# Optimization experiments

Hardware: AMD Instinct MI355X
Metric: run time of the kernel (lower is better)

## Reference

```python
import jax, jax.numpy as jnp
import numpy as np

DIM = 1024
HEADS = 16
HEAD_DIM = DIM // HEADS
HIDDEN = 4 * DIM
EPS = 1e-5


def layernorm(x, g, b):
    mu = jnp.mean(x, axis=-1, keepdims=True)
    var = jnp.var(x, axis=-1, keepdims=True)
    return (x - mu) * jax.lax.rsqrt(var + EPS) * g + b


def setup_inputs() -> dict:
    key = jax.random.key(0)
    ks = jax.random.split(key, 6)
    B, N = 4, 1024
    s = lambda fan_in: 1.0 / np.sqrt(fan_in)
    return {
        "x": jax.random.normal(ks[0], (B, N, DIM), jnp.float32),
        "ln1_g": jnp.ones((DIM,), jnp.float32),
        "ln1_b": jnp.zeros((DIM,), jnp.float32),
        "qkv_w": jax.random.normal(ks[1], (3 * DIM, DIM), jnp.float32) * s(DIM),
        "qkv_b": jnp.zeros((3 * DIM,), jnp.float32),
        "proj_w": jax.random.normal(ks[2], (DIM, DIM), jnp.float32) * s(DIM),
        "proj_b": jnp.zeros((DIM,), jnp.float32),
        "ln2_g": jnp.ones((DIM,), jnp.float32),
        "ln2_b": jnp.zeros((DIM,), jnp.float32),
        "fc1_w": jax.random.normal(ks[3], (HIDDEN, DIM), jnp.float32) * s(DIM),
        "fc1_b": jnp.zeros((HIDDEN,), jnp.float32),
        "fc2_w": jax.random.normal(ks[4], (DIM, HIDDEN), jnp.float32) * s(HIDDEN),
        "fc2_b": jnp.zeros((DIM,), jnp.float32),
    }


def reference(x, ln1_g, ln1_b, qkv_w, qkv_b, proj_w, proj_b,
              ln2_g, ln2_b, fc1_w, fc1_b, fc2_w, fc2_b):
    B, N, C = x.shape
    scale = HEAD_DIM ** -0.5

    # --- attention branch ---
    h = layernorm(x, ln1_g, ln1_b)
    qkv = h @ qkv_w.T + qkv_b                      # [B,N,3C]
    qkv = qkv.reshape(B, N, 3, HEADS, HEAD_DIM)
    q = qkv[:, :, 0].transpose(0, 2, 1, 3) * scale  # [B,H,N,D]
    k = qkv[:, :, 1].transpose(0, 2, 1, 3)
    v = qkv[:, :, 2].transpose(0, 2, 1, 3)
    attn = jax.nn.softmax(jnp.einsum('bhnd,bhmd->bhnm', q, k), axis=-1)
    o = jnp.einsum('bhnm,bhmd->bhnd', attn, v)      # [B,H,N,D]
    o = o.transpose(0, 2, 1, 3).reshape(B, N, C)
    x = x + (o @ proj_w.T + proj_b)

    # --- mlp branch ---
    h = layernorm(x, ln2_g, ln2_b)
    h = jax.nn.gelu(h @ fc1_w.T + fc1_b, approximate=False)
    x = x + (h @ fc2_w.T + fc2_b)
    return x
```

## Files before the change

### kernel.cpp

```cpp
#include <hip/hip_runtime.h>
#include <math.h>

#define DIM 1024
#define HEADS 16
#define HEAD_DIM 64
#define HIDDEN 4096
#define NSEQ 1024
#define BATCH 4
#define TOKENS (BATCH * NSEQ)
#define EPS 1e-5f

typedef __bf16 bf16;
typedef __bf16 bf16x4 __attribute__((ext_vector_type(4)));
typedef __bf16 bf16x8 __attribute__((ext_vector_type(8)));
typedef float f32x4 __attribute__((ext_vector_type(4)));

#define AS1 __attribute__((address_space(1)))
#define AS3 __attribute__((address_space(3)))

#define CVT_QUADS 3145728
#define CVT_BLOCKS 12288

__global__ __launch_bounds__(256) void prep_kernel(const float* __restrict__ x,
                                                   const float* __restrict__ g,
                                                   const float* __restrict__ bb,
                                                   bf16* __restrict__ h,
                                                   const float* __restrict__ s0,
                                                   const float* __restrict__ s1,
                                                   const float* __restrict__ s2,
                                                   const float* __restrict__ s3,
                                                   bf16* __restrict__ d0,
                                                   bf16* __restrict__ d1,
                                                   bf16* __restrict__ d2,
                                                   bf16* __restrict__ d3) {
    const int blk = blockIdx.x;
    const int tid = threadIdx.x;
    if (blk < CVT_BLOCKS) {
        size_t q = (size_t)blk * 256 + tid;
        const float* s;
        bf16* d;
        if (q < 786432) { s = s0; d = d0; }
        else if (q < 786432 + 262144) { q -= 786432; s = s1; d = d1; }
        else if (q < 786432 + 262144 + 1048576) { q -= 786432 + 262144; s = s2; d = d2; }
        else { q -= 786432 + 262144 + 1048576; s = s3; d = d3; }
        const float4 v = *(const float4*)(s + q * 4);
        bf16x4 o = {(bf16)v.x, (bf16)v.y, (bf16)v.z, (bf16)v.w};
        *(bf16x4*)(d + q * 4) = o;
        return;
    }
    const int t = blk - CVT_BLOCKS;
    const float* row = x + (size_t)t * DIM;
    float v[4];
    float s1v = 0.f, s2v = 0.f;
#pragma unroll
    for (int i = 0; i < 4; i++) {
        v[i] = row[tid + i * 256];
        s1v += v[i];
        s2v += v[i] * v[i];
    }
    __shared__ float w1[4], w2[4];
#pragma unroll
    for (int off = 32; off > 0; off >>= 1) {
        s1v += __shfl_down(s1v, off, 64);
        s2v += __shfl_down(s2v, off, 64);
    }
    const int wave = tid >> 6;
    if ((tid & 63) == 0) { w1[wave] = s1v; w2[wave] = s2v; }
    __syncthreads();
    const float sum = w1[0] + w1[1] + w1[2] + w1[3];
    const float ssq = w2[0] + w2[1] + w2[2] + w2[3];
    const float mu = sum * (1.0f / DIM);
    const float var = ssq * (1.0f / DIM) - mu * mu;
    const float rstd = rsqrtf(var + EPS);
    bf16* orow = h + (size_t)t * DIM;
#pragma unroll
    for (int i = 0; i < 4; i++) {
        const int idx = tid + i * 256;
        orow[idx] = (bf16)((v[i] - mu) * rstd * g[idx] + bb[idx]);
    }
}

__global__ __launch_bounds__(256) void ln_kernel(const float* __restrict__ x,
                                                 const float* __restrict__ g,
                                                 const float* __restrict__ b,
                                                 bf16* __restrict__ out) {
    const int t = blockIdx.x;
    const int tid = threadIdx.x;
    const float* row = x + (size_t)t * DIM;
    float v[4];
    float s1 = 0.f, s2 = 0.f;
#pragma unroll
    for (int i = 0; i < 4; i++) {
        v[i] = row[tid + i * 256];
        s1 += v[i];
        s2 += v[i] * v[i];
    }
    __shared__ float w1[4], w2[4];
#pragma unroll
    for (int off = 32; off > 0; off >>= 1) {
        s1 += __shfl_down(s1, off, 64);
        s2 += __shfl_down(s2, off, 64);
    }
    const int wave = tid >> 6;
    if ((tid & 63) == 0) { w1[wave] = s1; w2[wave] = s2; }
    __syncthreads();
    const float sum = w1[0] + w1[1] + w1[2] + w1[3];
    const float ssq = w2[0] + w2[1] + w2[2] + w2[3];
    const float mu = sum * (1.0f / DIM);
    const float var = ssq * (1.0f / DIM) - mu * mu;
    const float rstd = rsqrtf(var + EPS);
    bf16* orow = out + (size_t)t * DIM;
#pragma unroll
    for (int i = 0; i < 4; i++) {
        const int idx = tid + i * 256;
        orow[idx] = (bf16)((v[i] - mu) * rstd * g[idx] + b[idx]);
    }
}

#define ACT_NONE 0
#define ACT_GELU 1

template <int ACT, bool RES, bool OUT_BF16, bool VT, int SPLITK>
__global__ __launch_bounds__(256) void mfma_gemm(const bf16* __restrict__ A,
                                                 const bf16* __restrict__ W,
                                                 const float* __restrict__ bias,
                                                 const float* __restrict__ res,
                                                 void* __restrict__ Cout,
                                                 bf16* __restrict__ vTout,
                                                 int M, int N, int K) {
    __shared__ __align__(16) bf16 As[2][128 * 32];
    __shared__ __align__(16) bf16 Bs[2][128 * 32];

    const int tid = threadIdx.x;
    const int w = tid >> 6, lane = tid & 63;
    const int bm = blockIdx.y * 128, bn = blockIdx.x * 128;
    const int kseg = K / SPLITK;
    const int k0 = (SPLITK > 1) ? blockIdx.z * kseg : 0;

    const bf16* pa = A + (size_t)(bm + (tid >> 2)) * K + k0 + (tid & 3) * 8;
    const bf16* pb = W + (size_t)(bn + (tid >> 2)) * K + k0 + (tid & 3) * 8;
    const size_t rowskip = (size_t)64 * K;

    const int wm = (w & 1) * 64, wn = (w >> 1) * 64;
    const int fm = lane & 15, fk = (lane >> 4) * 8;
    const int foffA = (wm + fm) * 32 + fk;
    const int foffB = (wn + fm) * 32 + fk;

    f32x4 acc[4][4] = {};

    {
        char* lA = (char*)As[0] + (w << 10);
        char* lB = (char*)Bs[0] + (w << 10);
        __builtin_amdgcn_global_load_lds((const AS1 void*)pa, (AS3 void*)lA, 16, 0, 0);
        __builtin_amdgcn_global_load_lds((const AS1 void*)(pa + rowskip), (AS3 void*)(lA + 4096), 16, 0, 0);
        __builtin_amdgcn_global_load_lds((const AS1 void*)pb, (AS3 void*)lB, 16, 0, 0);
        __builtin_amdgcn_global_load_lds((const AS1 void*)(pb + rowskip), (AS3 void*)(lB + 4096), 16, 0, 0);
        pa += 32; pb += 32;
    }

    for (int kk = 0; kk < kseg; kk += 32) {
        const int p = (kk >> 5) & 1;
        __syncthreads();
        if (kk + 32 < kseg) {
            char* lA = (char*)As[p ^ 1] + (w << 10);
            char* lB = (char*)Bs[p ^ 1] + (w << 10);
            __builtin_amdgcn_global_load_lds((const AS1 void*)pa, (AS3 void*)lA, 16, 0, 0);
            __builtin_amdgcn_global_load_lds((const AS1 void*)(pa + rowskip), (AS3 void*)(lA + 4096), 16, 0, 0);
            __builtin_amdgcn_global_load_lds((const AS1 void*)pb, (AS3 void*)lB, 16, 0, 0);
            __builtin_amdgcn_global_load_lds((const AS1 void*)(pb + rowskip), (AS3 void*)(lB + 4096), 16, 0, 0);
            pa += 32; pb += 32;
        }
        const bf16* ab = As[p] + foffA;
        const bf16* bb = Bs[p] + foffB;
        bf16x8 af[4], bfr[4];
#pragma unroll
        for (int t = 0; t < 4; t++) af[t] = *(const bf16x8*)(ab + t * 16 * 32);
#pragma unroll
        for (int t = 0; t < 4; t++) bfr[t] = *(const bf16x8*)(bb + t * 16 * 32);
#pragma unroll
        for (int mt = 0; mt < 4; mt++)
#pragma unroll
            for (int nt = 0; nt < 4; nt++)
                acc[mt][nt] = __builtin_amdgcn_mfma_f32_16x16x32_bf16(af[mt], bfr[nt], acc[mt][nt], 0, 0, 0);
    }

    const int cn = bn + wn + fm;
    const int rm = bm + wm + (lane >> 4) * 4;
    float bv[4];
#pragma unroll
    for (int nt = 0; nt < 4; nt++)
        bv[nt] = (SPLITK > 1 && blockIdx.z != 0) ? 0.f : bias[cn + nt * 16];

    if (SPLITK > 1) {
        float* outp = (float*)Cout;
        const bool z0 = (blockIdx.z == 0);
#pragma unroll
        for (int mt = 0; mt < 4; mt++) {
#pragma unroll
            for (int r = 0; r < 4; r++) {
                const size_t rowoff = (size_t)(rm + mt * 16 + r) * N;
#pragma unroll
                for (int nt = 0; nt < 4; nt++) {
                    float val = acc[mt][nt][r] + bv[nt];
                    if (RES && z0) val += res[rowoff + cn + nt * 16];
                    atomicAdd(outp + rowoff + cn + nt * 16, val);
                }
            }
        }
        return;
    }

    if (VT && bn >= 2048) {
        const int dg0 = cn - 2048;
#pragma unroll
        for (int mt = 0; mt < 4; mt++) {
            const int mrow = rm + mt * 16;
            const int bI = mrow >> 10, j0 = mrow & 1023;
#pragma unroll
            for (int nt = 0; nt < 4; nt++) {
                const int dg = dg0 + nt * 16;
                bf16x4 v4 = {(bf16)(acc[mt][nt][0] + bv[nt]), (bf16)(acc[mt][nt][1] + bv[nt]),
                             (bf16)(acc[mt][nt][2] + bv[nt]), (bf16)(acc[mt][nt][3] + bv[nt])};
                *(bf16x4*)(vTout + ((size_t)(bI * 1024 + dg)) * 1024 + j0) = v4;
            }
        }
        return;
    }

#pragma unroll
    for (int mt = 0; mt < 4; mt++) {
#pragma unroll
        for (int r = 0; r < 4; r++) {
            const size_t rowoff = (size_t)(rm + mt * 16 + r) * N;
#pragma unroll
            for (int nt = 0; nt < 4; nt++) {
                float val = acc[mt][nt][r] + bv[nt];
                if (ACT == ACT_GELU) val = 0.5f * val * (1.0f + erff(val * 0.70710678118654752f));
                if (RES) val += res[rowoff + cn + nt * 16];
                if (OUT_BF16) ((bf16*)Cout)[rowoff + cn + nt * 16] = (bf16)val;
                else          ((float*)Cout)[rowoff + cn + nt * 16] = val;
            }
        }
    }
}

__global__ __launch_bounds__(256) void fattn_mfma(const bf16* __restrict__ qkv,
                                                  const bf16* __restrict__ vT,
                                                  bf16* __restrict__ out) {
    __shared__ __align__(16) bf16 Ks[64 * 64];
    __shared__ __align__(16) bf16 Vt[64 * 64];
    __shared__ __align__(16) bf16 Ps[64 * 68];

    const int bid = blockIdx.x;
    const int qt = bid & 15;
    const int h = (bid >> 4) & 15;
    const int b = bid >> 8;
    const int tid = threadIdx.x;
    const int w = tid >> 6, lane = tid & 63;
    const int li = lane & 15, g = lane >> 4;

    bf16x8 aQ[2];
    {
        const size_t tok = (size_t)b * NSEQ + qt * 64 + w * 16 + li;
#pragma unroll
        for (int ks = 0; ks < 2; ks++)
            aQ[ks] = *(const bf16x8*)(qkv + tok * (3 * DIM) + h * HEAD_DIM + g * 8 + 32 * ks);
    }

    float mrun[4] = {-INFINITY, -INFINITY, -INFINITY, -INFINITY};
    float lrun[4] = {0.f, 0.f, 0.f, 0.f};
    f32x4 o[4] = {};

    const int idx0 = w * 128 + lane;
    const int idx1 = idx0 + 64;
    const int jl0 = idx0 >> 3, c0 = (idx0 & 7) ^ (jl0 & 7);
    const int jl1 = idx1 >> 3, c1 = (idx1 & 7) ^ (jl1 & 7);
    bf16* ldsK0 = Ks + (size_t)(w * 128) * 8;
    bf16* ldsK1 = Ks + (size_t)(w * 128 + 64) * 8;
    bf16* ldsV0 = Vt + (size_t)(w * 128) * 8;
    bf16* ldsV1 = Vt + (size_t)(w * 128 + 64) * 8;
    const bf16* kbase = qkv + (size_t)b * NSEQ * (3 * DIM) + DIM + h * HEAD_DIM;
    const bf16* vbase = vT + ((size_t)b * DIM + h * HEAD_DIM) * NSEQ;

    for (int k0 = 0; k0 < NSEQ; k0 += 64) {
        __syncthreads();
        __builtin_amdgcn_global_load_lds((const AS1 void*)(kbase + (size_t)(k0 + jl0) * (3 * DIM) + c0 * 8),
                                         (AS3 void*)ldsK0, 16, 0, 0);
        __builtin_amdgcn_global_load_lds((const AS1 void*)(kbase + (size_t)(k0 + jl1) * (3 * DIM) + c1 * 8),
                                         (AS3 void*)ldsK1, 16, 0, 0);
        __builtin_amdgcn_global_load_lds((const AS1 void*)(vbase + (size_t)jl0 * NSEQ + k0 + c0 * 8),
                                         (AS3 void*)ldsV0, 16, 0, 0);
        __builtin_amdgcn_global_load_lds((const AS1 void*)(vbase + (size_t)jl1 * NSEQ + k0 + c1 * 8),
                                         (AS3 void*)ldsV1, 16, 0, 0);
        __syncthreads();

        f32x4 s[4] = {};
#pragma unroll
        for (int ks = 0; ks < 2; ks++) {
#pragma unroll
            for (int nt = 0; nt < 4; nt++) {
                const int j = li + 16 * nt;
                const int p = (g + 4 * ks) ^ (j & 7);
                bf16x8 bK = *(const bf16x8*)(Ks + j * 64 + p * 8);
                s[nt] = __builtin_amdgcn_mfma_f32_16x16x32_bf16(aQ[ks], bK, s[nt], 0, 0, 0);
            }
        }
#pragma unroll
        for (int nt = 0; nt < 4; nt++) s[nt] *= 0.125f;

        float m4[4], rs[4], alpha[4];
#pragma unroll
        for (int r = 0; r < 4; r++)
            m4[r] = fmaxf(fmaxf(s[0][r], s[1][r]), fmaxf(s[2][r], s[3][r]));
#pragma unroll
        for (int mask = 1; mask < 16; mask <<= 1)
#pragma unroll
            for (int r = 0; r < 4; r++) m4[r] = fmaxf(m4[r], __shfl_xor(m4[r], mask, 64));
#pragma unroll
        for (int r = 0; r < 4; r++) {
            const float mn = fmaxf(mrun[r], m4[r]);
            alpha[r] = __expf(mrun[r] - mn);
            mrun[r] = mn;
        }
#pragma unroll
        for (int r = 0; r < 4; r++) rs[r] = 0.f;
#pragma unroll
        for (int nt = 0; nt < 4; nt++) {
#pragma unroll
            for (int r = 0; r < 4; r++) {
                const float p = __expf(s[nt][r] - mrun[r]);
                rs[r] += p;
                Ps[(w * 16 + g * 4 + r) * 68 + li + 16 * nt] = (bf16)p;
            }
        }
#pragma unroll
        for (int mask = 1; mask < 16; mask <<= 1)
#pragma unroll
            for (int r = 0; r < 4; r++) rs[r] += __shfl_xor(rs[r], mask, 64);
#pragma unroll
        for (int r = 0; r < 4; r++) lrun[r] = lrun[r] * alpha[r] + rs[r];
#pragma unroll
        for (int nt = 0; nt < 4; nt++)
#pragma unroll
            for (int r = 0; r < 4; r++) o[nt][r] *= alpha[r];

        bf16x8 aP[2];
#pragma unroll
        for (int ks = 0; ks < 2; ks++) {
            const int off = (w * 16 + li) * 68 + g * 8 + 32 * ks;
            bf16x4 lo = *(const bf16x4*)(Ps + off);
            bf16x4 hi = *(const bf16x4*)(Ps + off + 4);
            aP[ks] = bf16x8{lo[0], lo[1], lo[2], lo[3], hi[0], hi[1], hi[2], hi[3]};
        }
#pragma unroll
        for (int ks = 0; ks < 2; ks++) {
#pragma unroll
            for (int nt = 0; nt < 4; nt++) {
                const int d = li + 16 * nt;
                const int p = (g + 4 * ks) ^ (d & 7);
                bf16x8 bV = *(const bf16x8*)(Vt + d * 64 + p * 8);
                o[nt] = __builtin_amdgcn_mfma_f32_16x16x32_bf16(aP[ks], bV, o[nt], 0, 0, 0);
            }
        }
    }

    float linv[4];
#pragma unroll
    for (int r = 0; r < 4; r++) linv[r] = 1.0f / lrun[r];
    const size_t tok0 = (size_t)b * NSEQ + qt * 64 + w * 16 + g * 4;
#pragma unroll
    for (int r = 0; r < 4; r++) {
#pragma unroll
        for (int nt = 0; nt < 4; nt++)
            out[(tok0 + r) * DIM + h * HEAD_DIM + 16 * nt + li] = (bf16)(o[nt][r] * linv[r]);
    }
}

extern "C" void kernel_launch(void* const* d_in, const int* in_sizes, int n_in,
                              void* d_out, int out_size, void* d_ws, size_t ws_size,
                              hipStream_t stream) {
    const float* x      = (const float*)d_in[0];
    const float* ln1_g  = (const float*)d_in[1];
    const float* ln1_b  = (const float*)d_in[2];
    const float* qkv_w  = (const float*)d_in[3];
    const float* qkv_b  = (const float*)d_in[4];
    const float* proj_w = (const float*)d_in[5];
    const float* proj_b = (const float*)d_in[6];
    const float* ln2_g  = (const float*)d_in[7];
    const float* ln2_b  = (const float*)d_in[8];
    const float* fc1_w  = (const float*)d_in[9];
    const float* fc1_b  = (const float*)d_in[10];
    const float* fc2_w  = (const float*)d_in[11];
    const float* fc2_b  = (const float*)d_in[12];
    float* out = (float*)d_out;

    char* p = (char*)d_ws;
    bf16*  h_bf    = (bf16*)p;  p += (size_t)TOKENS * DIM * 2;
    bf16*  attn_bf = (bf16*)p;  p += (size_t)TOKENS * DIM * 2;
    bf16*  ffn_bf  = (bf16*)p;  p += (size_t)TOKENS * HIDDEN * 2;
    bf16*  qkv_bf  = (bf16*)p;  p += (size_t)TOKENS * 3 * DIM * 2;
    bf16*  vT_bf   = (bf16*)p;  p += (size_t)BATCH * DIM * NSEQ * 2;
    bf16*  wq_bf   = (bf16*)p;  p += (size_t)3 * DIM * DIM * 2;
    bf16*  wp_bf   = (bf16*)p;  p += (size_t)DIM * DIM * 2;
    bf16*  w1_bf   = (bf16*)p;  p += (size_t)HIDDEN * DIM * 2;
    bf16*  w2_bf   = (bf16*)p;  p += (size_t)DIM * HIDDEN * 2;

    prep_kernel<<<CVT_BLOCKS + TOKENS, 256, 0, stream>>>(
        x, ln1_g, ln1_b, h_bf, qkv_w, proj_w, fc1_w, fc2_w, wq_bf, wp_bf, w1_bf, w2_bf);
    mfma_gemm<ACT_NONE, false, true, true, 1><<<dim3(3 * DIM / 128, TOKENS / 128), 256, 0, stream>>>(
        h_bf, wq_bf, qkv_b, nullptr, qkv_bf, vT_bf, TOKENS, 3 * DIM, DIM);
    fattn_mfma<<<BATCH * HEADS * (NSEQ / 64), 256, 0, stream>>>(qkv_bf, vT_bf, attn_bf);
    hipMemsetAsync(out, 0, (size_t)TOKENS * DIM * sizeof(float), stream);
    mfma_gemm<ACT_NONE, true, false, false, 4><<<dim3(DIM / 128, TOKENS / 128, 4), 256, 0, stream>>>(
        attn_bf, wp_bf, proj_b, x, out, nullptr, TOKENS, DIM, DIM);
    ln_kernel<<<TOKENS, 256, 0, stream>>>(out, ln2_g, ln2_b, h_bf);
    mfma_gemm<ACT_GELU, false, true, false, 1><<<dim3(HIDDEN / 128, TOKENS / 128), 256, 0, stream>>>(
        h_bf, w1_bf, fc1_b, nullptr, ffn_bf, nullptr, TOKENS, HIDDEN, DIM);
    mfma_gemm<ACT_NONE, false, false, false, 4><<<dim3(DIM / 128, TOKENS / 128, 4), 256, 0, stream>>>(
        ffn_bf, w2_bf, fc2_b, nullptr, out, nullptr, TOKENS, DIM, HIDDEN);
}
```

Baseline: 450.0 us.

## Replace split-K atomics with bf16 partial buffers reduced in fused epilogue kernels

The split-K GEMMs (proj and fc2) now write bf16 partial tiles to a scratch buffer that reuses the qkv region, instead of atomically adding fp32 into the output. A new ln2add kernel sums residual, partials and bias, writes the fp32 residual and LayerNorm2 in one pass, and an add2 kernel reduces the fc2 partials into the output. This removes the memset and the atomic traffic. The GEMM also drops LDS double-buffering for a single buffer with two barriers per K step, which shortens the load/compute overlap. Storing partials in bf16 loses some precision.

```diff
diff --git a/kernel.cpp b/kernel.cpp
--- a/kernel.cpp
+++ b/kernel.cpp
@@ -80,20 +80,27 @@
     }
 }
 
-__global__ __launch_bounds__(256) void ln_kernel(const float* __restrict__ x,
-                                                 const float* __restrict__ g,
-                                                 const float* __restrict__ b,
-                                                 bf16* __restrict__ out) {
+__global__ __launch_bounds__(256) void ln2add_kernel(const float* __restrict__ x,
+                                                     const bf16* __restrict__ p0,
+                                                     const bf16* __restrict__ p1,
+                                                     const float* __restrict__ pb,
+                                                     const float* __restrict__ g,
+                                                     const float* __restrict__ b,
+                                                     float* __restrict__ out,
+                                                     bf16* __restrict__ h2) {
     const int t = blockIdx.x;
     const int tid = threadIdx.x;
-    const float* row = x + (size_t)t * DIM;
+    const size_t base = (size_t)t * DIM;
     float v[4];
     float s1 = 0.f, s2 = 0.f;
 #pragma unroll
     for (int i = 0; i < 4; i++) {
-        v[i] = row[tid + i * 256];
-        s1 += v[i];
-        s2 += v[i] * v[i];
+        const int idx = tid + i * 256;
+        const float val = x[base + idx] + (float)p0[base + idx] + (float)p1[base + idx] + pb[idx];
+        v[i] = val;
+        out[base + idx] = val;
+        s1 += val;
+        s2 += val * val;
     }
     __shared__ float w1[4], w2[4];
 #pragma unroll
@@ -109,7 +116,7 @@
     const float mu = sum * (1.0f / DIM);
     const float var = ssq * (1.0f / DIM) - mu * mu;
     const float rstd = rsqrtf(var + EPS);
-    bf16* orow = out + (size_t)t * DIM;
+    bf16* orow = h2 + base;
 #pragma unroll
     for (int i = 0; i < 4; i++) {
         const int idx = tid + i * 256;
@@ -117,19 +124,40 @@
     }
 }
 
+__global__ __launch_bounds__(256) void add2_kernel(float* __restrict__ out,
+                                                   const bf16* __restrict__ q0,
+                                                   const bf16* __restrict__ q1,
+                                                   const bf16* __restrict__ q2,
+                                                   const bf16* __restrict__ q3,
+                                                   const float* __restrict__ bias) {
+    const size_t i = ((size_t)blockIdx.x * 256 + threadIdx.x) * 4;
+    const int col = (int)(i & (DIM - 1));
+    float4 o = *(const float4*)(out + i);
+    const float4 bv = *(const float4*)(bias + col);
+    bf16x4 a0 = *(const bf16x4*)(q0 + i);
+    bf16x4 a1 = *(const bf16x4*)(q1 + i);
+    bf16x4 a2 = *(const bf16x4*)(q2 + i);
+    bf16x4 a3 = *(const bf16x4*)(q3 + i);
+    o.x += (float)a0[0] + (float)a1[0] + (float)a2[0] + (float)a3[0] + bv.x;
+    o.y += (float)a0[1] + (float)a1[1] + (float)a2[1] + (float)a3[1] + bv.y;
+    o.z += (float)a0[2] + (float)a1[2] + (float)a2[2] + (float)a3[2] + bv.z;
+    o.w += (float)a0[3] + (float)a1[3] + (float)a2[3] + (float)a3[3] + bv.w;
+    *(float4*)(out + i) = o;
+}
+
 #define ACT_NONE 0
 #define ACT_GELU 1
 
-template <int ACT, bool RES, bool OUT_BF16, bool VT, int SPLITK>
+template <int ACT, bool OUT_BF16, bool VT, int SPLITK>
 __global__ __launch_bounds__(256) void mfma_gemm(const bf16* __restrict__ A,
                                                  const bf16* __restrict__ W,
                                                  const float* __restrict__ bias,
-                                                 const float* __restrict__ res,
                                                  void* __restrict__ Cout,
                                                  bf16* __restrict__ vTout,
+                                                 bf16* __restrict__ part,
                                                  int M, int N, int K) {
-    __shared__ __align__(16) bf16 As[2][128 * 32];
-    __shared__ __align__(16) bf16 Bs[2][128 * 32];
+    __shared__ __align__(16) bf16 As[128 * 32];
+    __shared__ __align__(16) bf16 Bs[128 * 32];
 
     const int tid = threadIdx.x;
     const int w = tid >> 6, lane = tid & 63;
@@ -140,75 +168,58 @@
     const bf16* pa = A + (size_t)(bm + (tid >> 2)) * K + k0 + (tid & 3) * 8;
     const bf16* pb = W + (size_t)(bn + (tid >> 2)) * K + k0 + (tid & 3) * 8;
     const size_t rowskip = (size_t)64 * K;
+    char* ldsA = (char*)As + (w << 10);
+    char* ldsB = (char*)Bs + (w << 10);
 
     const int wm = (w & 1) * 64, wn = (w >> 1) * 64;
     const int fm = lane & 15, fk = (lane >> 4) * 8;
-    const int foffA = (wm + fm) * 32 + fk;
-    const int foffB = (wn + fm) * 32 + fk;
+    const bf16* aoff = As + (wm + fm) * 32 + fk;
+    const bf16* boff = Bs + (wn + fm) * 32 + fk;
 
     f32x4 acc[4][4] = {};
 
-    {
-        char* lA = (char*)As[0] + (w << 10);
-        char* lB = (char*)Bs[0] + (w << 10);
-        __builtin_amdgcn_global_load_lds((const AS1 void*)pa, (AS3 void*)lA, 16, 0, 0);
-        __builtin_amdgcn_global_load_lds((const AS1 void*)(pa + rowskip), (AS3 void*)(lA + 4096), 16, 0, 0);
-        __builtin_amdgcn_global_load_lds((const AS1 void*)pb, (AS3 void*)lB, 16, 0, 0);
-        __builtin_amdgcn_global_load_lds((const AS1 void*)(pb + rowskip), (AS3 void*)(lB + 4096), 16, 0, 0);
+    for (int kk = 0; kk < kseg; kk += 32) {
+        __builtin_amdgcn_global_load_lds((const AS1 void*)pa, (AS3 void*)ldsA, 16, 0, 0);
+        __builtin_amdgcn_global_load_lds((const AS1 void*)(pa + rowskip), (AS3 void*)(ldsA + 4096), 16, 0, 0);
+        __builtin_amdgcn_global_load_lds((const AS1 void*)pb, (AS3 void*)ldsB, 16, 0, 0);
+        __builtin_amdgcn_global_load_lds((const AS1 void*)(pb + rowskip), (AS3 void*)(ldsB + 4096), 16, 0, 0);
         pa += 32; pb += 32;
-    }
-
-    for (int kk = 0; kk < kseg; kk += 32) {
-        const int p = (kk >> 5) & 1;
         __syncthreads();
-        if (kk + 32 < kseg) {
-            char* lA = (char*)As[p ^ 1] + (w << 10);
-            char* lB = (char*)Bs[p ^ 1] + (w << 10);
-            __builtin_amdgcn_global_load_lds((const AS1 void*)pa, (AS3 void*)lA, 16, 0, 0);
-            __builtin_amdgcn_global_load_lds((const AS1 void*)(pa + rowskip), (AS3 void*)(lA + 4096), 16, 0, 0);
-            __builtin_amdgcn_global_load_lds((const AS1 void*)pb, (AS3 void*)lB, 16, 0, 0);
-            __builtin_amdgcn_global_load_lds((const AS1 void*)(pb + rowskip), (AS3 void*)(lB + 4096), 16, 0, 0);
-            pa += 32; pb += 32;
-        }
-        const bf16* ab = As[p] + foffA;
-        const bf16* bb = Bs[p] + foffB;
+
         bf16x8 af[4], bfr[4];
 #pragma unroll
-        for (int t = 0; t < 4; t++) af[t] = *(const bf16x8*)(ab + t * 16 * 32);
-#pragma unroll
-        for (int t = 0; t < 4; t++) bfr[t] = *(const bf16x8*)(bb + t * 16 * 32);
+        for (int t = 0; t < 4; t++) af[t] = *(const bf16x8*)(aoff + t * 16 * 32);
+#pragma unroll
+        for (int t = 0; t < 4; t++) bfr[t] = *(const bf16x8*)(boff + t * 16 * 32);
 #pragma unroll
         for (int mt = 0; mt < 4; mt++)
 #pragma unroll
             for (int nt = 0; nt < 4; nt++)
                 acc[mt][nt] = __builtin_amdgcn_mfma_f32_16x16x32_bf16(af[mt], bfr[nt], acc[mt][nt], 0, 0, 0);
+        __syncthreads();
     }
 
     const int cn = bn + wn + fm;
     const int rm = bm + wm + (lane >> 4) * 4;
-    float bv[4];
-#pragma unroll
-    for (int nt = 0; nt < 4; nt++)
-        bv[nt] = (SPLITK > 1 && blockIdx.z != 0) ? 0.f : bias[cn + nt * 16];
 
     if (SPLITK > 1) {
-        float* outp = (float*)Cout;
-        const bool z0 = (blockIdx.z == 0);
+        bf16* pp = part + (size_t)blockIdx.z * M * N;
 #pragma unroll
         for (int mt = 0; mt < 4; mt++) {
 #pragma unroll
             for (int r = 0; r < 4; r++) {
                 const size_t rowoff = (size_t)(rm + mt * 16 + r) * N;
 #pragma unroll
-                for (int nt = 0; nt < 4; nt++) {
-                    float val = acc[mt][nt][r] + bv[nt];
-                    if (RES && z0) val += res[rowoff + cn + nt * 16];
-                    atomicAdd(outp + rowoff + cn + nt * 16, val);
-                }
+                for (int nt = 0; nt < 4; nt++)
+                    pp[rowoff + cn + nt * 16] = (bf16)acc[mt][nt][r];
             }
         }
         return;
     }
+
+    float bv[4];
+#pragma unroll
+    for (int nt = 0; nt < 4; nt++) bv[nt] = bias[cn + nt * 16];
 
     if (VT && bn >= 2048) {
         const int dg0 = cn - 2048;
@@ -236,7 +247,6 @@
             for (int nt = 0; nt < 4; nt++) {
                 float val = acc[mt][nt][r] + bv[nt];
                 if (ACT == ACT_GELU) val = 0.5f * val * (1.0f + erff(val * 0.70710678118654752f));
-                if (RES) val += res[rowoff + cn + nt * 16];
                 if (OUT_BF16) ((bf16*)Cout)[rowoff + cn + nt * 16] = (bf16)val;
                 else          ((float*)Cout)[rowoff + cn + nt * 16] = val;
             }
@@ -404,18 +414,23 @@
     bf16*  wp_bf   = (bf16*)p;  p += (size_t)DIM * DIM * 2;
     bf16*  w1_bf   = (bf16*)p;  p += (size_t)HIDDEN * DIM * 2;
     bf16*  w2_bf   = (bf16*)p;  p += (size_t)DIM * HIDDEN * 2;
+    bf16*  proj_part = qkv_bf;
+    bf16*  fc2_part  = qkv_bf;
 
     prep_kernel<<<CVT_BLOCKS + TOKENS, 256, 0, stream>>>(
         x, ln1_g, ln1_b, h_bf, qkv_w, proj_w, fc1_w, fc2_w, wq_bf, wp_bf, w1_bf, w2_bf);
-    mfma_gemm<ACT_NONE, false, true, true, 1><<<dim3(3 * DIM / 128, TOKENS / 128), 256, 0, stream>>>(
-        h_bf, wq_bf, qkv_b, nullptr, qkv_bf, vT_bf, TOKENS, 3 * DIM, DIM);
+    mfma_gemm<ACT_NONE, true, true, 1><<<dim3(3 * DIM / 128, TOKENS / 128), 256, 0, stream>>>(
+        h_bf, wq_bf, qkv_b, qkv_bf, vT_bf, nullptr, TOKENS, 3 * DIM, DIM);
     fattn_mfma<<<BATCH * HEADS * (NSEQ / 64), 256, 0, stream>>>(qkv_bf, vT_bf, attn_bf);
-    hipMemsetAsync(out, 0, (size_t)TOKENS * DIM * sizeof(float), stream);
-    mfma_gemm<ACT_NONE, true, false, false, 4><<<dim3(DIM / 128, TOKENS / 128, 4), 256, 0, stream>>>(
-        attn_bf, wp_bf, proj_b, x, out, nullptr, TOKENS, DIM, DIM);
-    ln_kernel<<<TOKENS, 256, 0, stream>>>(out, ln2_g, ln2_b, h_bf);
-    mfma_gemm<ACT_GELU, false, true, false, 1><<<dim3(HIDDEN / 128, TOKENS / 128), 256, 0, stream>>>(
-        h_bf, w1_bf, fc1_b, nullptr, ffn_bf, nullptr, TOKENS, HIDDEN, DIM);
-    mfma_gemm<ACT_NONE, false, false, false, 4><<<dim3(DIM / 128, TOKENS / 128, 4), 256, 0, stream>>>(
-        ffn_bf, w2_bf, fc2_b, nullptr, out, nullptr, TOKENS, DIM, HIDDEN);
-}
+    mfma_gemm<ACT_NONE, false, false, 2><<<dim3(DIM / 128, TOKENS / 128, 2), 256, 0, stream>>>(
+        attn_bf, wp_bf, proj_b, nullptr, nullptr, proj_part, TOKENS, DIM, DIM);
+    ln2add_kernel<<<TOKENS, 256, 0, stream>>>(
+        x, proj_part, proj_part + (size_t)TOKENS * DIM, proj_b, ln2_g, ln2_b, out, h_bf);
+    mfma_gemm<ACT_GELU, true, false, 1><<<dim3(HIDDEN / 128, TOKENS / 128), 256, 0, stream>>>(
+        h_bf, w1_bf, fc1_b, ffn_bf, nullptr, nullptr, TOKENS, HIDDEN, DIM);
+    mfma_gemm<ACT_NONE, false, false, 4><<<dim3(DIM / 128, TOKENS / 128, 4), 256, 0, stream>>>(
+        ffn_bf, w2_bf, fc2_b, nullptr, nullptr, fc2_part, TOKENS, DIM, HIDDEN);
+    add2_kernel<<<TOKENS * DIM / 1024, 256, 0, stream>>>(
+        out, fc2_part, fc2_part + (size_t)TOKENS * DIM, fc2_part + (size_t)2 * TOKENS * DIM,
+        fc2_part + (size_t)3 * TOKENS * DIM, fc2_b);
+}
```

Result: faster. 399.7 us (-11.2%).
